# Kernel optimization log

Measured on AMD Instinct MI355X. Metric: run time of the kernel, lower is better.

Reference implementation:

```python
import jax, jax.numpy as jnp
import numpy as np

B, S, DM = 4, 4096, 1024
H, DH = 16, 64          # num_attention_heads, attention_head_size
K = 128                 # Linformer projection dim (k_dims)


def setup_inputs() -> dict:
    key = jax.random.key(0)
    ks = jax.random.split(key, 9)
    s = 1.0 / np.sqrt(DM)
    return {
        "hidden_states": jax.random.normal(ks[0], (B, S, DM), jnp.float32),
        "Wq": jax.random.normal(ks[1], (DM, DM), jnp.float32) * s,
        "bq": jax.random.normal(ks[2], (DM,), jnp.float32) * 0.02,
        "Wk": jax.random.normal(ks[3], (DM, DM), jnp.float32) * s,
        "bk": jax.random.normal(ks[4], (DM,), jnp.float32) * 0.02,
        "Wv": jax.random.normal(ks[5], (DM, DM), jnp.float32) * s,
        "bv": jax.random.normal(ks[6], (DM,), jnp.float32) * 0.02,
        # E, D: [k_dims, max_input_len], init randn/sqrt(k_dims) as in torch module
        "E": jax.random.normal(ks[7], (K, S), jnp.float32) / np.sqrt(K),
        "D": jax.random.normal(ks[8], (K, S), jnp.float32) / np.sqrt(K),
    }


def reference(hidden_states, Wq, bq, Wk, bk, Wv, bv, E, D):
    b, s, _ = hidden_states.shape

    def heads(x):  # [b,s,DM] -> [b,H,s,DH]
        return x.reshape(b, s, H, DH).transpose(0, 2, 1, 3)

    # torch Linear: y = x @ W.T + b
    q = heads(hidden_states @ Wq.T + bq)   # [b,H,s,DH]
    k = heads(hidden_states @ Wk.T + bk)   # [b,H,s,DH]
    v = heads(hidden_states @ Wv.T + bv)   # [b,H,s,DH]

    # Linformer low-rank projection along the sequence axis
    pk = jnp.einsum('ks,bhsd->bhkd', E[:, :s], k)  # [b,H,K,DH]
    pv = jnp.einsum('ks,bhsd->bhkd', D[:, :s], v)  # [b,H,K,DH]

    scores = jnp.einsum('bhsd,bhkd->bhsk', q, pk) / np.sqrt(DH).astype(np.float32)
    probs = jax.nn.softmax(scores, axis=-1)        # [b,H,s,K]
    ctx = jnp.einsum('bhsk,bhkd->bhsd', probs, pv) # [b,H,s,DH]
    return ctx.transpose(0, 2, 1, 3).reshape(b, s, H * DH)
```

## Files before the change

kernel.cpp:

```cpp
#include <hip/hip_runtime.h>
#include <hip/hip_bf16.h>
#include <stdint.h>


typedef __attribute__((ext_vector_type(8))) _Float16 f16x8;
typedef __attribute__((ext_vector_type(4))) _Float16 f16x4;
typedef __attribute__((ext_vector_type(4))) float    f32x4;

__device__ __forceinline__ f32x4 mfma16(f16x8 a, f16x8 b, f32x4 c) {
    return __builtin_amdgcn_mfma_f32_16x16x32_f16(a, b, c, 0, 0, 0);
}

__device__ __forceinline__ void gload16(const void* g, void* l) {
    __builtin_amdgcn_global_load_lds(
        (const __attribute__((address_space(1))) void*)g,
        (__attribute__((address_space(3))) void*)l, 16, 0, 0);
}

__global__ __launch_bounds__(256) void cvt_f16(const float* __restrict__ in,
                                               _Float16* __restrict__ out, int n4) {
    int i = blockIdx.x * 256 + threadIdx.x;
    int stride = gridDim.x * 256;
    for (; i < n4; i += stride) {
        f32x4 v = reinterpret_cast<const f32x4*>(in)[i];
        f16x4 o;
#pragma unroll
        for (int j = 0; j < 4; ++j) o[j] = (_Float16)v[j];
        reinterpret_cast<f16x4*>(out)[i] = o;
    }
}

__global__ __launch_bounds__(256) void cvt_f16_2(const float* __restrict__ in0,
                                                 _Float16* __restrict__ out0,
                                                 const float* __restrict__ in1,
                                                 _Float16* __restrict__ out1, int n4) {
    const float* in = blockIdx.y ? in1 : in0;
    _Float16* out = blockIdx.y ? out1 : out0;
    int i = blockIdx.x * 256 + threadIdx.x;
    int stride = gridDim.x * 256;
    for (; i < n4; i += stride) {
        f32x4 v = reinterpret_cast<const f32x4*>(in)[i];
        f16x4 o;
#pragma unroll
        for (int j = 0; j < 4; ++j) o[j] = (_Float16)v[j];
        reinterpret_cast<f16x4*>(out)[i] = o;
    }
}

__global__ __launch_bounds__(256) void cvt_hilo2(const float* __restrict__ in0,
                                                 _Float16* __restrict__ hi0,
                                                 _Float16* __restrict__ lo0,
                                                 const float* __restrict__ in1,
                                                 _Float16* __restrict__ hi1,
                                                 _Float16* __restrict__ lo1, int n4) {
    const float* in = blockIdx.y ? in1 : in0;
    _Float16* hi = blockIdx.y ? hi1 : hi0;
    _Float16* lo = blockIdx.y ? lo1 : lo0;
    int i = blockIdx.x * 256 + threadIdx.x;
    int stride = gridDim.x * 256;
    for (; i < n4; i += stride) {
        f32x4 v = reinterpret_cast<const f32x4*>(in)[i];
        f16x4 h, l;
#pragma unroll
        for (int j = 0; j < 4; ++j) {
            _Float16 hb = (_Float16)v[j];
            h[j] = hb;
            l[j] = (_Float16)(v[j] - (float)hb);
        }
        reinterpret_cast<f16x4*>(hi)[i] = h;
        reinterpret_cast<f16x4*>(lo)[i] = l;
    }
}

__global__ __launch_bounds__(256) void rowsum_k(const float* __restrict__ E,
                                                const float* __restrict__ D,
                                                float* __restrict__ sE,
                                                float* __restrict__ sD) {
    __shared__ float red[256];
    const int blk = blockIdx.x;
    const float* src = (blk < 128) ? E : D;
    float* dst = (blk < 128) ? sE : sD;
    const int row = blk & 127;
    float s = 0.f;
    for (int i = threadIdx.x; i < 4096; i += 256) s += src[(size_t)row * 4096 + i];
    red[threadIdx.x] = s;
    __syncthreads();
    for (int off = 128; off > 0; off >>= 1) {
        if ((int)threadIdx.x < off) red[threadIdx.x] += red[threadIdx.x + off];
        __syncthreads();
    }
    if (threadIdx.x == 0) dst[row] = red[0];
}

__global__ __launch_bounds__(512) void gemm_q_f16(
    const _Float16* __restrict__ A, const _Float16* __restrict__ B,
    const float* __restrict__ bias, _Float16* __restrict__ Q) {
    const int Kd = 1024, N = 1024, NT = 16;
    __shared__ _Float16 Asm[2][256 * 64];
    __shared__ _Float16 Bsm[2][256 * 64];
    const int tid = threadIdx.x, lane = tid & 63, wave = tid >> 6;
    const int l15 = lane & 15, lg = lane >> 4;
    const int row0 = blockIdx.x * 256, col0 = blockIdx.y * 256;
    const int wr = (wave >> 2) * 128, wc = (wave & 3) * 64;
    f32x4 acc[8][4];
#pragma unroll
    for (int m = 0; m < 8; ++m)
#pragma unroll
        for (int n = 0; n < 4; ++n) acc[m][n] = (f32x4)0.0f;

    const _Float16* aSrc[4];
    const _Float16* bSrc[4];
    int ub[4];
#pragma unroll
    for (int it = 0; it < 4; ++it) {
        int u = it * 512 + tid;
        int r = u >> 3, c = u & 7;
        int sc = (c ^ (r & 7)) * 8;
        aSrc[it] = A + (size_t)(row0 + r) * Kd + sc;
        bSrc[it] = B + (size_t)(col0 + r) * Kd + sc;
        ub[it] = it * 512 + wave * 64;
    }
    auto stage = [&](int buf, int t) {
        const int k0 = t * 64;
#pragma unroll
        for (int it = 0; it < 4; ++it)
            gload16(aSrc[it] + k0, &Asm[buf][ub[it] * 8]);
#pragma unroll
        for (int it = 0; it < 4; ++it)
            gload16(bSrc[it] + k0, &Bsm[buf][ub[it] * 8]);
    };

    stage(0, 0);
#pragma unroll 1
    for (int t = 0; t < NT; ++t) {
        const int cur = t & 1;
        if (t < NT - 1) {
            stage(cur ^ 1, t + 1);
            asm volatile("s_waitcnt vmcnt(8)" ::: "memory");
        } else {
            asm volatile("s_waitcnt vmcnt(0)" ::: "memory");
        }
        __builtin_amdgcn_s_barrier();
#pragma unroll
        for (int kk = 0; kk < 2; ++kk) {
            const int ksw = ((kk * 4 + lg) ^ (l15 & 7)) * 8;
            f16x8 af[8], bfr[4];
#pragma unroll
            for (int m = 0; m < 8; ++m)
                af[m] = *reinterpret_cast<const f16x8*>(
                    &Asm[cur][(wr + m * 16 + l15) * 64 + ksw]);
#pragma unroll
            for (int n = 0; n < 4; ++n)
                bfr[n] = *reinterpret_cast<const f16x8*>(
                    &Bsm[cur][(wc + n * 16 + l15) * 64 + ksw]);
#pragma unroll
            for (int m = 0; m < 8; ++m)
#pragma unroll
                for (int n = 0; n < 4; ++n) acc[m][n] = mfma16(af[m], bfr[n], acc[m][n]);
        }
        __builtin_amdgcn_s_barrier();
    }
#pragma unroll
    for (int m = 0; m < 8; ++m)
#pragma unroll
        for (int n = 0; n < 4; ++n) {
            int colg = col0 + wc + n * 16 + l15;
            float bi = bias[colg];
#pragma unroll
            for (int r = 0; r < 4; ++r) {
                int rowg = row0 + wr + m * 16 + lg * 4 + r;
                Q[(size_t)rowg * N + colg] = (_Float16)(acc[m][n][r] + bi);
            }
        }
}

__global__ __launch_bounds__(256) void eproj2(const _Float16* __restrict__ EB,
                                              const _Float16* __restrict__ DB,
                                              const _Float16* __restrict__ X,
                                              float* __restrict__ EHf,
                                              float* __restrict__ DHf) {
    __shared__ _Float16 Ea[128 * 72];
    __shared__ _Float16 BT[128 * 72];
    const int tid = threadIdx.x, lane = tid & 63, wave = tid >> 6;
    const int l15 = lane & 15, lg = lane >> 4;
    const int sc = blockIdx.x;
    const int n0 = blockIdx.y * 128;
    const int bb = blockIdx.z & 3;
    const _Float16* Emat = (blockIdx.z >> 2) ? DB : EB;
    float* Of = (blockIdx.z >> 2) ? DHf : EHf;
    const int wr = (wave >> 1) * 64, wc = (wave & 1) * 64;
    const int nb = tid & 31, sb = tid >> 5;
    f32x4 acc[4][4];
#pragma unroll
    for (int m = 0; m < 4; ++m)
#pragma unroll
        for (int n = 0; n < 4; ++n) acc[m][n] = (f32x4)0.0f;

    for (int ks = 0; ks < 512; ks += 64) {
        const int s0 = sc * 512 + ks;
        __syncthreads();
#pragma unroll
        for (int i = 0; i < 4; ++i) {
            int u = tid + 256 * i;
            int r = u >> 3, c8 = (u & 7) * 8;
            *reinterpret_cast<f16x8*>(&Ea[r * 72 + c8]) =
                *reinterpret_cast<const f16x8*>(Emat + (size_t)r * 4096 + s0 + c8);
        }
        {
            f16x4 rr[8];
#pragma unroll
            for (int i = 0; i < 8; ++i)
                rr[i] = *reinterpret_cast<const f16x4*>(
                    X + (size_t)(bb * 4096 + s0 + sb * 8 + i) * 1024 + n0 + nb * 4);
#pragma unroll
            for (int j = 0; j < 4; ++j) {
                f16x8 w;
#pragma unroll
                for (int i = 0; i < 8; ++i) w[i] = rr[i][j];
                *reinterpret_cast<f16x8*>(&BT[(nb * 4 + j) * 72 + sb * 8]) = w;
            }
        }
        __syncthreads();
#pragma unroll
        for (int kk = 0; kk < 2; ++kk) {
            f16x8 af[4], bfr[4];
#pragma unroll
            for (int m = 0; m < 4; ++m)
                af[m] = *reinterpret_cast<const f16x8*>(
                    &Ea[(wr + m * 16 + l15) * 72 + kk * 32 + lg * 8]);
#pragma unroll
            for (int n = 0; n < 4; ++n)
                bfr[n] = *reinterpret_cast<const f16x8*>(
                    &BT[(wc + n * 16 + l15) * 72 + kk * 32 + lg * 8]);
#pragma unroll
            for (int m = 0; m < 4; ++m)
#pragma unroll
                for (int n = 0; n < 4; ++n) acc[m][n] = mfma16(af[m], bfr[n], acc[m][n]);
        }
    }
#pragma unroll
    for (int m = 0; m < 4; ++m)
#pragma unroll
        for (int n = 0; n < 4; ++n)
#pragma unroll
            for (int r = 0; r < 4; ++r)
                atomicAdd(&Of[(size_t)(bb * 128 + wr + m * 16 + lg * 4 + r) * 1024 +
                              n0 + wc + n * 16 + l15],
                          acc[m][n][r]);
}

__global__ __launch_bounds__(256) void gemm_split2(
    const float* __restrict__ A0, const _Float16* __restrict__ Bh0,
    const _Float16* __restrict__ Bl0, const float* __restrict__ bias0,
    const float* __restrict__ rs0, _Float16* __restrict__ PKH,
    const float* __restrict__ A1, const _Float16* __restrict__ Bh1,
    const _Float16* __restrict__ Bl1, const float* __restrict__ bias1,
    const float* __restrict__ rs1, _Float16* __restrict__ PVT) {
    const int Kd = 1024;
    const float* A = blockIdx.z ? A1 : A0;
    const _Float16* Bh = blockIdx.z ? Bh1 : Bh0;
    const _Float16* Bl = blockIdx.z ? Bl1 : Bl0;
    const float* bias = blockIdx.z ? bias1 : bias0;
    const float* rowscale = blockIdx.z ? rs1 : rs0;
    __shared__ _Float16 Ah[64 * 40], Al[64 * 40], Bhs[64 * 40], Bls[64 * 40];
    const int tid = threadIdx.x, lane = tid & 63, wave = tid >> 6;
    const int l15 = lane & 15, lg = lane >> 4;
    const int row0 = blockIdx.x * 64, col0 = blockIdx.y * 64;
    const int wr = (wave >> 1) * 32, wc = (wave & 1) * 32;
    f32x4 acc[2][2];
#pragma unroll
    for (int m = 0; m < 2; ++m)
#pragma unroll
        for (int n = 0; n < 2; ++n) acc[m][n] = (f32x4)0.0f;

    const int r = tid >> 2, c8 = (tid & 3) * 8;
    for (int k0 = 0; k0 < Kd; k0 += 32) {
        __syncthreads();
        {
            const float* src = A + (size_t)(row0 + r) * Kd + k0 + c8;
            f32x4 v0 = *reinterpret_cast<const f32x4*>(src);
            f32x4 v1 = *reinterpret_cast<const f32x4*>(src + 4);
            f16x8 h8, l8;
#pragma unroll
            for (int j = 0; j < 4; ++j) {
                _Float16 hb = (_Float16)v0[j];
                h8[j] = hb; l8[j] = (_Float16)(v0[j] - (float)hb);
            }
#pragma unroll
            for (int j = 0; j < 4; ++j) {
                _Float16 hb = (_Float16)v1[j];
                h8[4 + j] = hb; l8[4 + j] = (_Float16)(v1[j] - (float)hb);
            }
            *reinterpret_cast<f16x8*>(&Ah[r * 40 + c8]) = h8;
            *reinterpret_cast<f16x8*>(&Al[r * 40 + c8]) = l8;
            *reinterpret_cast<f16x8*>(&Bhs[r * 40 + c8]) =
                *reinterpret_cast<const f16x8*>(Bh + (size_t)(col0 + r) * Kd + k0 + c8);
            *reinterpret_cast<f16x8*>(&Bls[r * 40 + c8]) =
                *reinterpret_cast<const f16x8*>(Bl + (size_t)(col0 + r) * Kd + k0 + c8);
        }
        __syncthreads();
        f16x8 ah[2], al[2], bh[2], bl[2];
#pragma unroll
        for (int m = 0; m < 2; ++m) {
            ah[m] = *reinterpret_cast<const f16x8*>(&Ah[(wr + m * 16 + l15) * 40 + lg * 8]);
            al[m] = *reinterpret_cast<const f16x8*>(&Al[(wr + m * 16 + l15) * 40 + lg * 8]);
        }
#pragma unroll
        for (int n = 0; n < 2; ++n) {
            bh[n] = *reinterpret_cast<const f16x8*>(&Bhs[(wc + n * 16 + l15) * 40 + lg * 8]);
            bl[n] = *reinterpret_cast<const f16x8*>(&Bls[(wc + n * 16 + l15) * 40 + lg * 8]);
        }
#pragma unroll
        for (int m = 0; m < 2; ++m)
#pragma unroll
            for (int n = 0; n < 2; ++n) {
                acc[m][n] = mfma16(ah[m], bh[n], acc[m][n]);
                acc[m][n] = mfma16(al[m], bh[n], acc[m][n]);
                acc[m][n] = mfma16(ah[m], bl[n], acc[m][n]);
            }
    }
#pragma unroll
    for (int m = 0; m < 2; ++m)
#pragma unroll
        for (int n = 0; n < 2; ++n) {
            int colg = col0 + wc + n * 16 + l15;
            float bi = bias[colg];
#pragma unroll
            for (int rr2 = 0; rr2 < 4; ++rr2) {
                int rowg = row0 + wr + m * 16 + lg * 4 + rr2;
                float val = acc[m][n][rr2] + rowscale[rowg & 127] * bi;
                if (blockIdx.z == 0) {
                    PKH[(size_t)rowg * 1024 + colg] = (_Float16)(val * 0.125f);
                } else {
                    PVT[(size_t)((rowg >> 7) * 16 + (colg >> 6)) * 8192 +
                        (colg & 63) * 128 + (rowg & 127)] = (_Float16)val;
                }
            }
        }
}

__global__ __launch_bounds__(256, 4) void attn_fused(
    const _Float16* __restrict__ QH, const _Float16* __restrict__ PKH,
    const _Float16* __restrict__ PVT, float* __restrict__ Out) {
    __shared__ _Float16 smem[16384];
    const int tid = threadIdx.x, lane = tid & 63, wave = tid >> 6;
    const int l15 = lane & 15, lg = lane >> 4;
    const int st = blockIdx.x, h = blockIdx.y, bb = blockIdx.z;

    {
        const _Float16* pkh_g = PKH + (size_t)(bb * 128) * 1024 + h * 64;
        const _Float16* pvt_g = PVT + (size_t)(bb * 16 + h) * 8192;
        const int su = wave * 64 + lane;
#pragma unroll
        for (int it = 0; it < 4; ++it) {
            int u = it * 256 + su;
            int ub = it * 256 + wave * 64;
            {
                int r = u >> 3, c = u & 7;
                int sc = (c ^ (r & 7)) * 8;
                gload16(pkh_g + (size_t)r * 1024 + sc, &smem[ub * 8]);
            }
            {
                int r = u >> 4, c = u & 15;
                int sc = (c ^ (r & 7)) * 8;
                gload16(pvt_g + r * 128 + sc, &smem[8192 + ub * 8]);
            }
        }
    }
    const int srow0 = bb * 4096 + st * 128 + wave * 32;
    f16x8 qf[2][2];
#pragma unroll
    for (int m = 0; m < 2; ++m)
#pragma unroll
        for (int kk = 0; kk < 2; ++kk)
            qf[m][kk] = *reinterpret_cast<const f16x8*>(
                QH + (size_t)(srow0 + m * 16 + l15) * 1024 + h * 64 + kk * 32 + lg * 8);
    __syncthreads();

    f32x4 accT[8][2];
#pragma unroll
    for (int n = 0; n < 8; ++n)
#pragma unroll
        for (int m = 0; m < 2; ++m) accT[n][m] = (f32x4)0.0f;
#pragma unroll
    for (int kk = 0; kk < 2; ++kk)
#pragma unroll
        for (int n = 0; n < 8; ++n) {
            f16x8 pk = *reinterpret_cast<const f16x8*>(
                &smem[(n * 16 + l15) * 64 + (((kk * 4 + lg) ^ (l15 & 7)) * 8)]);
#pragma unroll
            for (int m = 0; m < 2; ++m)
                accT[n][m] = mfma16(pk, qf[m][kk], accT[n][m]);
        }
    __syncthreads();

#pragma unroll
    for (int m = 0; m < 2; ++m) {
        float v = -1e30f;
#pragma unroll
        for (int n = 0; n < 8; ++n)
#pragma unroll
            for (int r = 0; r < 4; ++r) v = fmaxf(v, accT[n][m][r]);
        v = fmaxf(v, __shfl_xor(v, 16));
        v = fmaxf(v, __shfl_xor(v, 32));
        float s = 0.f;
#pragma unroll
        for (int n = 0; n < 8; ++n)
#pragma unroll
            for (int r = 0; r < 4; ++r) {
                float e = __expf(accT[n][m][r] - v);
                accT[n][m][r] = e;
                s += e;
            }
        s += __shfl_xor(s, 16);
        s += __shfl_xor(s, 32);
        float inv = 1.0f / s;
#pragma unroll
        for (int n = 0; n < 8; ++n)
#pragma unroll
            for (int r = 0; r < 4; ++r) accT[n][m][r] *= inv;
    }

    _Float16* pw = smem + wave * 2048;
    f32x4 o[2][4];
#pragma unroll
    for (int m = 0; m < 2; ++m)
#pragma unroll
        for (int n = 0; n < 4; ++n) o[m][n] = (f32x4)0.0f;
#pragma unroll
    for (int half = 0; half < 2; ++half) {
#pragma unroll
        for (int nl = 0; nl < 4; ++nl) {
            int n = half * 4 + nl;
#pragma unroll
            for (int m = 0; m < 2; ++m) {
                int q = l15 + 16 * m;
                int kp = (nl * 8 + lg * 2) ^ ((q & 7) << 2);
                f16x4 v;
#pragma unroll
                for (int r = 0; r < 4; ++r) v[r] = (_Float16)accT[n][m][r];
                *reinterpret_cast<f16x4*>(&pw[q * 64 + kp * 2]) = v;
            }
        }
#pragma unroll
        for (int ksl = 0; ksl < 2; ++ksl) {
            f16x8 pa[2];
#pragma unroll
            for (int m = 0; m < 2; ++m) {
                int q = m * 16 + l15;
                int kpb = (ksl * 16 + lg * 4) ^ ((q & 7) << 2);
                pa[m] = *reinterpret_cast<const f16x8*>(&pw[q * 64 + kpb * 2]);
            }
            int ks = half * 2 + ksl;
#pragma unroll
            for (int n = 0; n < 4; ++n) {
                int dd = n * 16 + l15;
                f16x8 bv = *reinterpret_cast<const f16x8*>(
                    &smem[8192 + dd * 128 + (((ks * 4 + lg) ^ (dd & 7)) * 8)]);
#pragma unroll
                for (int m = 0; m < 2; ++m) o[m][n] = mfma16(pa[m], bv, o[m][n]);
            }
        }
    }

#pragma unroll
    for (int m = 0; m < 2; ++m)
#pragma unroll
        for (int n = 0; n < 4; ++n)
#pragma unroll
            for (int r = 0; r < 4; ++r) {
                int row = srow0 + m * 16 + lg * 4 + r;
                Out[(size_t)row * 1024 + h * 64 + n * 16 + l15] = o[m][n][r];
            }
}

extern "C" void kernel_launch(void* const* d_in, const int* in_sizes, int n_in,
                              void* d_out, int out_size, void* d_ws, size_t ws_size,
                              hipStream_t stream) {
    const float* hs = (const float*)d_in[0];
    const float* Wq = (const float*)d_in[1];
    const float* bq = (const float*)d_in[2];
    const float* Wk = (const float*)d_in[3];
    const float* bk = (const float*)d_in[4];
    const float* Wv = (const float*)d_in[5];
    const float* bv = (const float*)d_in[6];
    const float* Em = (const float*)d_in[7];
    const float* Dm = (const float*)d_in[8];
    float* out = (float*)d_out;
    char* ws = (char*)d_ws;

    _Float16* hsB = (_Float16*)(ws + 0);
    _Float16* WqB = (_Float16*)(ws + 33554432);
    _Float16* WkH = (_Float16*)(ws + 35651584);
    _Float16* WkL = (_Float16*)(ws + 37748736);
    _Float16* WvH = (_Float16*)(ws + 39845888);
    _Float16* WvL = (_Float16*)(ws + 41943040);
    _Float16* EB  = (_Float16*)(ws + 44040192);
    _Float16* DB  = (_Float16*)(ws + 45088768);
    float* sE  = (float*)(ws + 46137344);
    float* sD  = (float*)(ws + 46137856);
    _Float16* QHq = (_Float16*)(ws + 46138368);
    float* EHf = (float*)(ws + 113247232);
    float* DHf = (float*)(ws + 115344384);
    _Float16* PKH = (_Float16*)(ws + 117441536);
    _Float16* PVT = (_Float16*)(ws + 118490112);

    cvt_f16<<<2048, 256, 0, stream>>>(hs, hsB, 16777216 / 4);
    cvt_f16<<<1024, 256, 0, stream>>>(Wq, WqB, 1048576 / 4);
    cvt_hilo2<<<dim3(1024, 2), 256, 0, stream>>>(Wk, WkH, WkL, Wv, WvH, WvL,
                                                 1048576 / 4);
    cvt_f16_2<<<dim3(512, 2), 256, 0, stream>>>(Em, EB, Dm, DB, 524288 / 4);
    rowsum_k<<<256, 256, 0, stream>>>(Em, Dm, sE, sD);
    gemm_q_f16<<<dim3(64, 4), 512, 0, stream>>>(hsB, WqB, bq, QHq);
    hipMemsetAsync(EHf, 0, 2 * 512 * 1024 * sizeof(float), stream);
    eproj2<<<dim3(8, 8, 8), 256, 0, stream>>>(EB, DB, hsB, EHf, DHf);
    gemm_split2<<<dim3(8, 16, 2), 256, 0, stream>>>(EHf, WkH, WkL, bk, sE, PKH,
                                                    DHf, WvH, WvL, bv, sD, PVT);
    attn_fused<<<dim3(32, 16, 4), 256, 0, stream>>>(QHq, PKH, PVT, out);
}
```

Measured before the change: 164.0 us.

## Interleave next-tile global loads with MFMA phases in projection GEMM loop

Splits each k-tile iteration of the projection GEMM into four phases. Each phase issues a slice of the next tile's global-to-LDS loads, then runs half of a k-step's MFMAs, so memory traffic is spread across the compute instead of issued in one burst. MFMA sections are wrapped in s_setprio to favor the math waves. The cost is a block barrier after every phase, four times as many as before, plus reduced B-fragment register use.

```diff
diff --git a/kernel.cpp b/kernel.cpp
--- a/kernel.cpp
+++ b/kernel.cpp
@@ -120,45 +120,52 @@
         bSrc[it] = B + (size_t)(col0 + r) * Kd + sc;
         ub[it] = it * 512 + wave * 64;
     }
-    auto stage = [&](int buf, int t) {
-        const int k0 = t * 64;
-#pragma unroll
-        for (int it = 0; it < 4; ++it)
-            gload16(aSrc[it] + k0, &Asm[buf][ub[it] * 8]);
-#pragma unroll
-        for (int it = 0; it < 4; ++it)
-            gload16(bSrc[it] + k0, &Bsm[buf][ub[it] * 8]);
-    };
-
-    stage(0, 0);
+#pragma unroll
+    for (int it = 0; it < 4; ++it) gload16(aSrc[it], &Asm[0][ub[it] * 8]);
+#pragma unroll
+    for (int it = 0; it < 4; ++it) gload16(bSrc[it], &Bsm[0][ub[it] * 8]);
+
 #pragma unroll 1
     for (int t = 0; t < NT; ++t) {
         const int cur = t & 1;
-        if (t < NT - 1) {
-            stage(cur ^ 1, t + 1);
-            asm volatile("s_waitcnt vmcnt(8)" ::: "memory");
-        } else {
-            asm volatile("s_waitcnt vmcnt(0)" ::: "memory");
-        }
-        __builtin_amdgcn_s_barrier();
-#pragma unroll
-        for (int kk = 0; kk < 2; ++kk) {
+        const _Float16* As = Asm[cur];
+        const _Float16* Bs = Bsm[cur];
+        f16x8 af[8];
+#pragma unroll
+        for (int ph = 0; ph < 4; ++ph) {
+            const int kk = ph >> 1, nh = ph & 1;
+            if (t < NT - 1) {
+                const int k0 = (t + 1) * 64;
+                gload16(aSrc[ph] + k0, &Asm[cur ^ 1][ub[ph] * 8]);
+                gload16(bSrc[ph] + k0, &Bsm[cur ^ 1][ub[ph] * 8]);
+            }
+            if (ph == 0) {
+                if (t < NT - 1)
+                    asm volatile("s_waitcnt vmcnt(2)" ::: "memory");
+                else
+                    asm volatile("s_waitcnt vmcnt(0)" ::: "memory");
+            }
+            __builtin_amdgcn_s_barrier();
             const int ksw = ((kk * 4 + lg) ^ (l15 & 7)) * 8;
-            f16x8 af[8], bfr[4];
-#pragma unroll
-            for (int m = 0; m < 8; ++m)
-                af[m] = *reinterpret_cast<const f16x8*>(
-                    &Asm[cur][(wr + m * 16 + l15) * 64 + ksw]);
-#pragma unroll
-            for (int n = 0; n < 4; ++n)
-                bfr[n] = *reinterpret_cast<const f16x8*>(
-                    &Bsm[cur][(wc + n * 16 + l15) * 64 + ksw]);
-#pragma unroll
-            for (int m = 0; m < 8; ++m)
-#pragma unroll
-                for (int n = 0; n < 4; ++n) acc[m][n] = mfma16(af[m], bfr[n], acc[m][n]);
-        }
-        __builtin_amdgcn_s_barrier();
+            if (nh == 0) {
+#pragma unroll
+                for (int m = 0; m < 8; ++m)
+                    af[m] = *reinterpret_cast<const f16x8*>(
+                        &As[(wr + m * 16 + l15) * 64 + ksw]);
+            }
+            f16x8 b0 = *reinterpret_cast<const f16x8*>(
+                &Bs[(wc + (nh * 2) * 16 + l15) * 64 + ksw]);
+            f16x8 b1 = *reinterpret_cast<const f16x8*>(
+                &Bs[(wc + (nh * 2 + 1) * 16 + l15) * 64 + ksw]);
+            __builtin_amdgcn_s_setprio(1);
+#pragma unroll
+            for (int m = 0; m < 8; ++m) {
+                acc[m][nh * 2] = mfma16(af[m], b0, acc[m][nh * 2]);
+                acc[m][nh * 2 + 1] = mfma16(af[m], b1, acc[m][nh * 2 + 1]);
+            }
+            __builtin_amdgcn_s_setprio(0);
+            __builtin_amdgcn_s_barrier();
+        }
     }
 #pragma unroll
     for (int m = 0; m < 8; ++m)
```

Result: slower. 177.0 us (+8.0%).
